# Optimization experiments

Measured on AMD Instinct MI355X. Metric: run time of the kernel, lower is better.

Reference implementation:

```python
import jax, jax.numpy as jnp
import numpy as np


def setup_inputs() -> dict:
    key = jax.random.key(0)
    ks = jax.random.split(key, 5)
    B, T, S = 64, 128, 1024
    IN_DIM, OUT_DIM = 1024, 1024
    decoder_output = jax.random.normal(ks[0], (B, T, OUT_DIM), dtype=jnp.float32)
    encoder_outputs = jax.random.normal(ks[1], (B, S, IN_DIM), dtype=jnp.float32)
    encoder_padding_mask = jax.random.randint(ks[2], (B, S), 0, 2).astype(bool)
    # nn.Linear(output_dim, input_dim, bias=False): weight [input_dim, output_dim]
    W_attn = jax.random.normal(ks[3], (IN_DIM, OUT_DIM), dtype=jnp.float32) * (1.0 / np.sqrt(OUT_DIM))
    # nn.Linear(input_dim+output_dim, output_dim): weight [output_dim, input_dim+output_dim]
    W_out = jax.random.normal(ks[4], (OUT_DIM, IN_DIM + OUT_DIM), dtype=jnp.float32) * (1.0 / np.sqrt(IN_DIM + OUT_DIM))
    b_out = jnp.zeros((OUT_DIM,), dtype=jnp.float32)
    return {"decoder_output": decoder_output, "encoder_outputs": encoder_outputs,
            "encoder_padding_mask": encoder_padding_mask,
            "W_attn": W_attn, "W_out": W_out, "b_out": b_out}


def reference(decoder_output, encoder_outputs, encoder_padding_mask, W_attn, W_out, b_out):
    # general score: bmm(attn(query), key^T)
    q_proj = jnp.einsum('bto,io->bti', decoder_output, W_attn)          # [B,T,in_dim]
    scores = jnp.einsum('bti,bsi->bts', q_proj, encoder_outputs)        # [B,T,S]
    scores = jnp.where(encoder_padding_mask[:, None, :], -jnp.inf, scores)
    attn_weights = jax.nn.softmax(scores, axis=-1)                      # [B,T,S]
    context = jnp.einsum('bts,bsi->bti', attn_weights, encoder_outputs) # [B,T,in_dim]
    cat = jnp.concatenate([context, decoder_output], axis=-1)           # [B,T,in+out]
    attn_outputs = jnp.tanh(jnp.einsum('btc,oc->bto', cat, W_out) + b_out)
    return attn_outputs, attn_weights
```

## Files before the change

kernel.cpp:

```cpp
#include <hip/hip_runtime.h>
#include <math.h>


#define LSTR 40

typedef __attribute__((ext_vector_type(8))) short short8;
typedef __attribute__((ext_vector_type(4))) float f32x4;
typedef __attribute__((ext_vector_type(4))) unsigned short u16x4;

__device__ __forceinline__ unsigned short f2bf(float x) {
    union { float f; unsigned int u; } v; v.f = x;
    unsigned int u = v.u + (0x7fffu + ((v.u >> 16) & 1u));
    return (unsigned short)(u >> 16);
}
__device__ __forceinline__ float bf2f(unsigned short h) {
    union { unsigned int u; float f; } v; v.u = ((unsigned int)h) << 16;
    return v.f;
}

__global__ __launch_bounds__(256) void gemm_bt_split(
    const float* __restrict__ A, const float* __restrict__ B, float* __restrict__ C,
    int N, int K, long long sA, long long sB, long long sC)
{
    const float* Ab = A + blockIdx.z * sA;
    const float* Bb = B + blockIdx.z * sB;
    float*       Cb = C + blockIdx.z * sC;
    const int m0 = blockIdx.x * 128, n0 = blockIdx.y * 128;

    __shared__ unsigned short Ah[128*LSTR], Al[128*LSTR], Bh[128*LSTR], Bl[128*LSTR];

    const int tid = threadIdx.x;
    const int lane = tid & 63, wave = tid >> 6;
    const int wm = (wave & 1) * 64, wn = (wave >> 1) * 64;
    const int fr = lane & 15, kq = lane >> 4;

    f32x4 zero = {0.f, 0.f, 0.f, 0.f};
    f32x4 acc[4][4];
    #pragma unroll
    for (int i = 0; i < 4; i++)
        #pragma unroll
        for (int j = 0; j < 4; j++) acc[i][j] = zero;

    for (int k0 = 0; k0 < K; k0 += 32) {
        #pragma unroll
        for (int i = 0; i < 4; i++) {
            int f = i * 256 + tid;
            int row = f >> 3, c4 = (f & 7) * 4;
            float4 a4 = *(const float4*)(Ab + (long long)(m0 + row) * K + k0 + c4);
            float4 b4 = *(const float4*)(Bb + (long long)(n0 + row) * K + k0 + c4);
            float av[4] = {a4.x, a4.y, a4.z, a4.w};
            float bv[4] = {b4.x, b4.y, b4.z, b4.w};
            u16x4 ah, al, bh, bl;
            #pragma unroll
            for (int j = 0; j < 4; j++) {
                unsigned short h = f2bf(av[j]);
                ah[j] = h; al[j] = f2bf(av[j] - bf2f(h));
                h = f2bf(bv[j]);
                bh[j] = h; bl[j] = f2bf(bv[j] - bf2f(h));
            }
            *(u16x4*)&Ah[row*LSTR + c4] = ah;
            *(u16x4*)&Al[row*LSTR + c4] = al;
            *(u16x4*)&Bh[row*LSTR + c4] = bh;
            *(u16x4*)&Bl[row*LSTR + c4] = bl;
        }
        __syncthreads();

        short8 fah[4], fal[4], fbh[4], fbl[4];
        #pragma unroll
        for (int fi = 0; fi < 4; fi++) {
            fah[fi] = *(const short8*)&Ah[(wm + fi*16 + fr)*LSTR + kq*8];
            fal[fi] = *(const short8*)&Al[(wm + fi*16 + fr)*LSTR + kq*8];
            fbh[fi] = *(const short8*)&Bh[(wn + fi*16 + fr)*LSTR + kq*8];
            fbl[fi] = *(const short8*)&Bl[(wn + fi*16 + fr)*LSTR + kq*8];
        }
        #pragma unroll
        for (int fi = 0; fi < 4; fi++)
            #pragma unroll
            for (int fj = 0; fj < 4; fj++) {
                acc[fi][fj] = __builtin_amdgcn_mfma_f32_16x16x32_bf16(fah[fi], fbh[fj], acc[fi][fj], 0, 0, 0);
                acc[fi][fj] = __builtin_amdgcn_mfma_f32_16x16x32_bf16(fah[fi], fbl[fj], acc[fi][fj], 0, 0, 0);
                acc[fi][fj] = __builtin_amdgcn_mfma_f32_16x16x32_bf16(fal[fi], fbh[fj], acc[fi][fj], 0, 0, 0);
            }
        __syncthreads();
    }

    #pragma unroll
    for (int fi = 0; fi < 4; fi++) {
        int rb = m0 + wm + fi*16 + kq*4;
        #pragma unroll
        for (int fj = 0; fj < 4; fj++) {
            int col = n0 + wn + fj*16 + fr;
            #pragma unroll
            for (int j = 0; j < 4; j++)
                Cb[(long long)(rb + j) * N + col] = acc[fi][fj][j];
        }
    }
}

__global__ __launch_bounds__(256) void softmax_mask(
    float* __restrict__ sw, const int* __restrict__ mask,
    unsigned short* __restrict__ wbf)
{
    const int row = blockIdx.x;
    const int b = row >> 7;
    const int tid = threadIdx.x, lane = tid & 63, wave = tid >> 6;
    float* sr = sw + (long long)row * 1024;
    const int* mr = mask + (long long)b * 1024;

    float4 x = *(const float4*)(sr + tid * 4);
    int4  mk = *(const int4*)(mr + tid * 4);
    float v0 = mk.x ? -INFINITY : x.x;
    float v1 = mk.y ? -INFINITY : x.y;
    float v2 = mk.z ? -INFINITY : x.z;
    float v3 = mk.w ? -INFINITY : x.w;

    float mx = fmaxf(fmaxf(v0, v1), fmaxf(v2, v3));
    #pragma unroll
    for (int off = 32; off; off >>= 1) mx = fmaxf(mx, __shfl_xor(mx, off));
    __shared__ float redm[4];
    __shared__ float reds[4];
    if (lane == 0) redm[wave] = mx;
    __syncthreads();
    mx = fmaxf(fmaxf(redm[0], redm[1]), fmaxf(redm[2], redm[3]));

    float p0 = __expf(v0 - mx), p1 = __expf(v1 - mx);
    float p2 = __expf(v2 - mx), p3 = __expf(v3 - mx);
    float s = (p0 + p1) + (p2 + p3);
    #pragma unroll
    for (int off = 32; off; off >>= 1) s += __shfl_xor(s, off);
    if (lane == 0) reds[wave] = s;
    __syncthreads();
    s = (reds[0] + reds[1]) + (reds[2] + reds[3]);
    float inv = 1.0f / s;

    float w0 = p0*inv, w1 = p1*inv, w2 = p2*inv, w3 = p3*inv;
    float4 w4; w4.x = w0; w4.y = w1; w4.z = w2; w4.w = w3;
    *(float4*)(sr + tid * 4) = w4;
    u16x4 wb; wb[0] = f2bf(w0); wb[1] = f2bf(w1); wb[2] = f2bf(w2); wb[3] = f2bf(w3);
    *(u16x4*)(wbf + (long long)row * 1024 + tid * 4) = wb;
}

__global__ __launch_bounds__(256) void gemm_ctx(
    const unsigned short* __restrict__ Wb, const float* __restrict__ enc,
    unsigned short* __restrict__ cat)
{
    const int bz = blockIdx.z;
    const int n0 = blockIdx.y * 128;
    const unsigned short* Ab = Wb + (long long)bz * 128 * 1024;
    const float* Bb = enc + (long long)bz * 1024 * 1024;

    __shared__ unsigned short Ah[128*LSTR], Bh[128*LSTR];

    const int tid = threadIdx.x, lane = tid & 63, wave = tid >> 6;
    const int wm = (wave & 1) * 64, wn = (wave >> 1) * 64;
    const int fr = lane & 15, kq = lane >> 4;

    f32x4 zero = {0.f, 0.f, 0.f, 0.f};
    f32x4 acc[4][4];
    #pragma unroll
    for (int i = 0; i < 4; i++)
        #pragma unroll
        for (int j = 0; j < 4; j++) acc[i][j] = zero;

    for (int k0 = 0; k0 < 1024; k0 += 32) {
        #pragma unroll
        for (int i = 0; i < 2; i++) {
            int f = i * 256 + tid;
            int row = f >> 2, c8 = (f & 3) * 8;
            *(short8*)&Ah[row*LSTR + c8] = *(const short8*)(Ab + (long long)row*1024 + k0 + c8);
        }
        #pragma unroll
        for (int jj = 0; jj < 16; jj++) {
            int linear = jj * 256 + tid;
            int kr = linear >> 7, n = linear & 127;
            Bh[n*LSTR + kr] = f2bf(Bb[(long long)(k0 + kr) * 1024 + n0 + n]);
        }
        __syncthreads();

        short8 fa[4], fb[4];
        #pragma unroll
        for (int fi = 0; fi < 4; fi++) {
            fa[fi] = *(const short8*)&Ah[(wm + fi*16 + fr)*LSTR + kq*8];
            fb[fi] = *(const short8*)&Bh[(wn + fi*16 + fr)*LSTR + kq*8];
        }
        #pragma unroll
        for (int fi = 0; fi < 4; fi++)
            #pragma unroll
            for (int fj = 0; fj < 4; fj++)
                acc[fi][fj] = __builtin_amdgcn_mfma_f32_16x16x32_bf16(fa[fi], fb[fj], acc[fi][fj], 0, 0, 0);
        __syncthreads();
    }

    #pragma unroll
    for (int fi = 0; fi < 4; fi++) {
        int rb = bz * 128 + wm + fi*16 + kq*4;
        #pragma unroll
        for (int fj = 0; fj < 4; fj++) {
            int col = n0 + wn + fj*16 + fr;
            #pragma unroll
            for (int j = 0; j < 4; j++)
                cat[(long long)(rb + j) * 2048 + col] = f2bf(acc[fi][fj][j]);
        }
    }
}

__global__ __launch_bounds__(256) void pack_dec(
    const float* __restrict__ dec, unsigned short* __restrict__ cat)
{
    long long i = (long long)blockIdx.x * 256 + threadIdx.x;
    float4 x = *(const float4*)(dec + i * 4);
    long long e = i * 4;
    int m = (int)(e >> 10), c = (int)(e & 1023);
    u16x4 h; h[0] = f2bf(x.x); h[1] = f2bf(x.y); h[2] = f2bf(x.z); h[3] = f2bf(x.w);
    *(u16x4*)(cat + (long long)m * 2048 + 1024 + c) = h;
}

__global__ __launch_bounds__(256) void gemm_out(
    const unsigned short* __restrict__ cat, const float* __restrict__ W,
    const float* __restrict__ bias, float* __restrict__ out)
{
    const int m0 = blockIdx.x * 128, n0 = blockIdx.y * 128;

    __shared__ unsigned short Ah[128*LSTR], Bh[128*LSTR];

    const int tid = threadIdx.x, lane = tid & 63, wave = tid >> 6;
    const int wm = (wave & 1) * 64, wn = (wave >> 1) * 64;
    const int fr = lane & 15, kq = lane >> 4;

    f32x4 zero = {0.f, 0.f, 0.f, 0.f};
    f32x4 acc[4][4];
    #pragma unroll
    for (int i = 0; i < 4; i++)
        #pragma unroll
        for (int j = 0; j < 4; j++) acc[i][j] = zero;

    for (int k0 = 0; k0 < 2048; k0 += 32) {
        #pragma unroll
        for (int i = 0; i < 2; i++) {
            int f = i * 256 + tid;
            int row = f >> 2, c8 = (f & 3) * 8;
            *(short8*)&Ah[row*LSTR + c8] = *(const short8*)(cat + (long long)(m0 + row)*2048 + k0 + c8);
        }
        #pragma unroll
        for (int i = 0; i < 4; i++) {
            int f = i * 256 + tid;
            int row = f >> 3, c4 = (f & 7) * 4;
            float4 b4 = *(const float4*)(W + (long long)(n0 + row)*2048 + k0 + c4);
            u16x4 bh; bh[0] = f2bf(b4.x); bh[1] = f2bf(b4.y); bh[2] = f2bf(b4.z); bh[3] = f2bf(b4.w);
            *(u16x4*)&Bh[row*LSTR + c4] = bh;
        }
        __syncthreads();

        short8 fa[4], fb[4];
        #pragma unroll
        for (int fi = 0; fi < 4; fi++) {
            fa[fi] = *(const short8*)&Ah[(wm + fi*16 + fr)*LSTR + kq*8];
            fb[fi] = *(const short8*)&Bh[(wn + fi*16 + fr)*LSTR + kq*8];
        }
        #pragma unroll
        for (int fi = 0; fi < 4; fi++)
            #pragma unroll
            for (int fj = 0; fj < 4; fj++)
                acc[fi][fj] = __builtin_amdgcn_mfma_f32_16x16x32_bf16(fa[fi], fb[fj], acc[fi][fj], 0, 0, 0);
        __syncthreads();
    }

    #pragma unroll
    for (int fi = 0; fi < 4; fi++) {
        int rb = m0 + wm + fi*16 + kq*4;
        #pragma unroll
        for (int fj = 0; fj < 4; fj++) {
            int col = n0 + wn + fj*16 + fr;
            float bb = bias[col];
            #pragma unroll
            for (int j = 0; j < 4; j++)
                out[(long long)(rb + j) * 1024 + col] = tanhf(acc[fi][fj][j] + bb);
        }
    }
}

extern "C" void kernel_launch(void* const* d_in, const int* in_sizes, int n_in,
                              void* d_out, int out_size, void* d_ws, size_t ws_size,
                              hipStream_t stream) {
    const float* dec    = (const float*)d_in[0];
    const float* enc    = (const float*)d_in[1];
    const int*   mask   = (const int*)d_in[2];
    const float* W_attn = (const float*)d_in[3];
    const float* W_out  = (const float*)d_in[4];
    const float* b_out  = (const float*)d_in[5];

    float* out_attn = (float*)d_out;
    float* weights  = out_attn + 8388608;

    char* ws = (char*)d_ws;
    float*          q_proj = (float*)ws;
    unsigned short* w_bf   = (unsigned short*)(ws + (32 << 20));
    unsigned short* cat    = (unsigned short*)(ws + (48 << 20));

    dim3 blk(256);

    gemm_bt_split<<<dim3(64, 8, 1), blk, 0, stream>>>(
        dec, W_attn, q_proj, 1024, 1024, 0, 0, 0);

    gemm_bt_split<<<dim3(1, 8, 64), blk, 0, stream>>>(
        q_proj, enc, weights, 1024, 1024, 128LL*1024, 1024LL*1024, 128LL*1024);

    softmax_mask<<<dim3(8192), blk, 0, stream>>>(weights, mask, w_bf);

    pack_dec<<<dim3(8192), blk, 0, stream>>>(dec, cat);

    gemm_ctx<<<dim3(1, 8, 64), blk, 0, stream>>>(w_bf, enc, cat);

    gemm_out<<<dim3(64, 8, 1), blk, 0, stream>>>(cat, W_out, b_out, out_attn);
}
```

Baseline: 679.3 us.

## Pre-split operands to bf16 hi/lo, use direct global-to-LDS loads, vectorize ctx transpose

Adds separate kernels that convert dec, W_attn and W_out to bf16 (hi/lo pairs where needed) once, so the GEMMs no longer convert inside their K loops. The GEMMs then stage their bf16 tiles with global_load_lds straight into unpadded LDS, and q_proj is stored as bf16 hi/lo instead of fp32. gemm_ctx replaces its scalar transposed encoder loads with float4 loads and a register transpose. gemm_out now reads ctx and dec_hi directly, so the pack_dec kernel is gone. The cost is extra conversion kernels, more workspace traffic, and possible LDS bank conflicts from dropping the row padding.

```diff
diff --git a/kernel.cpp b/kernel.cpp
--- a/kernel.cpp
+++ b/kernel.cpp
@@ -1,8 +1,6 @@
 #include <hip/hip_runtime.h>
 #include <math.h>
 
-
-#define LSTR 40
 
 typedef __attribute__((ext_vector_type(8))) short short8;
 typedef __attribute__((ext_vector_type(4))) float f32x4;
@@ -17,22 +15,50 @@
     union { unsigned int u; float f; } v; v.u = ((unsigned int)h) << 16;
     return v.f;
 }
-
-__global__ __launch_bounds__(256) void gemm_bt_split(
-    const float* __restrict__ A, const float* __restrict__ B, float* __restrict__ C,
-    int N, int K, long long sA, long long sB, long long sC)
-{
-    const float* Ab = A + blockIdx.z * sA;
-    const float* Bb = B + blockIdx.z * sB;
-    float*       Cb = C + blockIdx.z * sC;
+__device__ __forceinline__ void g2lds16(const void* g, void* l) {
+    __builtin_amdgcn_global_load_lds(
+        (const __attribute__((address_space(1))) void*)g,
+        (__attribute__((address_space(3))) void*)l, 16, 0, 0);
+}
+
+__global__ __launch_bounds__(256) void split_f32(
+    const float* __restrict__ src, unsigned short* __restrict__ hi,
+    unsigned short* __restrict__ lo)
+{
+    long long i = (long long)blockIdx.x * 256 + threadIdx.x;
+    float4 x = *(const float4*)(src + i * 4);
+    float v[4] = {x.x, x.y, x.z, x.w};
+    u16x4 h, l;
+    #pragma unroll
+    for (int j = 0; j < 4; j++) {
+        h[j] = f2bf(v[j]);
+        l[j] = f2bf(v[j] - bf2f(h[j]));
+    }
+    *(u16x4*)(hi + i * 4) = h;
+    *(u16x4*)(lo + i * 4) = l;
+}
+
+__global__ __launch_bounds__(256) void cvt_f32(
+    const float* __restrict__ src, unsigned short* __restrict__ dst)
+{
+    long long i = (long long)blockIdx.x * 256 + threadIdx.x;
+    float4 x = *(const float4*)(src + i * 4);
+    u16x4 h; h[0] = f2bf(x.x); h[1] = f2bf(x.y); h[2] = f2bf(x.z); h[3] = f2bf(x.w);
+    *(u16x4*)(dst + i * 4) = h;
+}
+
+__global__ __launch_bounds__(256) void gemm3_qproj(
+    const unsigned short* __restrict__ Ahi, const unsigned short* __restrict__ Alo,
+    const unsigned short* __restrict__ Bhi, const unsigned short* __restrict__ Blo,
+    unsigned short* __restrict__ Chi, unsigned short* __restrict__ Clo)
+{
     const int m0 = blockIdx.x * 128, n0 = blockIdx.y * 128;
-
-    __shared__ unsigned short Ah[128*LSTR], Al[128*LSTR], Bh[128*LSTR], Bl[128*LSTR];
-
-    const int tid = threadIdx.x;
-    const int lane = tid & 63, wave = tid >> 6;
+    __shared__ __align__(16) unsigned short Ah[128*32], Al[128*32], Bh[128*32], Bl[128*32];
+
+    const int tid = threadIdx.x, lane = tid & 63, wave = tid >> 6;
     const int wm = (wave & 1) * 64, wn = (wave >> 1) * 64;
     const int fr = lane & 15, kq = lane >> 4;
+    const int row0 = tid >> 2, c80 = (tid & 3) * 8;
 
     f32x4 zero = {0.f, 0.f, 0.f, 0.f};
     f32x4 acc[4][4];
@@ -41,37 +67,28 @@
         #pragma unroll
         for (int j = 0; j < 4; j++) acc[i][j] = zero;
 
-    for (int k0 = 0; k0 < K; k0 += 32) {
-        #pragma unroll
-        for (int i = 0; i < 4; i++) {
-            int f = i * 256 + tid;
-            int row = f >> 3, c4 = (f & 7) * 4;
-            float4 a4 = *(const float4*)(Ab + (long long)(m0 + row) * K + k0 + c4);
-            float4 b4 = *(const float4*)(Bb + (long long)(n0 + row) * K + k0 + c4);
-            float av[4] = {a4.x, a4.y, a4.z, a4.w};
-            float bv[4] = {b4.x, b4.y, b4.z, b4.w};
-            u16x4 ah, al, bh, bl;
-            #pragma unroll
-            for (int j = 0; j < 4; j++) {
-                unsigned short h = f2bf(av[j]);
-                ah[j] = h; al[j] = f2bf(av[j] - bf2f(h));
-                h = f2bf(bv[j]);
-                bh[j] = h; bl[j] = f2bf(bv[j] - bf2f(h));
-            }
-            *(u16x4*)&Ah[row*LSTR + c4] = ah;
-            *(u16x4*)&Al[row*LSTR + c4] = al;
-            *(u16x4*)&Bh[row*LSTR + c4] = bh;
-            *(u16x4*)&Bl[row*LSTR + c4] = bl;
-        }
+    for (int k0 = 0; k0 < 1024; k0 += 32) {
+        const unsigned short* pa = Ahi + (long long)(m0 + row0) * 1024 + k0 + c80;
+        const unsigned short* pl = Alo + (long long)(m0 + row0) * 1024 + k0 + c80;
+        const unsigned short* pb = Bhi + (long long)(n0 + row0) * 1024 + k0 + c80;
+        const unsigned short* pm = Blo + (long long)(n0 + row0) * 1024 + k0 + c80;
+        g2lds16(pa,            &Ah[tid*8]);
+        g2lds16(pa + 64*1024,  &Ah[tid*8 + 2048]);
+        g2lds16(pl,            &Al[tid*8]);
+        g2lds16(pl + 64*1024,  &Al[tid*8 + 2048]);
+        g2lds16(pb,            &Bh[tid*8]);
+        g2lds16(pb + 64*1024,  &Bh[tid*8 + 2048]);
+        g2lds16(pm,            &Bl[tid*8]);
+        g2lds16(pm + 64*1024,  &Bl[tid*8 + 2048]);
         __syncthreads();
 
         short8 fah[4], fal[4], fbh[4], fbl[4];
         #pragma unroll
         for (int fi = 0; fi < 4; fi++) {
-            fah[fi] = *(const short8*)&Ah[(wm + fi*16 + fr)*LSTR + kq*8];
-            fal[fi] = *(const short8*)&Al[(wm + fi*16 + fr)*LSTR + kq*8];
-            fbh[fi] = *(const short8*)&Bh[(wn + fi*16 + fr)*LSTR + kq*8];
-            fbl[fi] = *(const short8*)&Bl[(wn + fi*16 + fr)*LSTR + kq*8];
+            fah[fi] = *(const short8*)&Ah[(wm + fi*16 + fr)*32 + kq*8];
+            fal[fi] = *(const short8*)&Al[(wm + fi*16 + fr)*32 + kq*8];
+            fbh[fi] = *(const short8*)&Bh[(wn + fi*16 + fr)*32 + kq*8];
+            fbl[fi] = *(const short8*)&Bl[(wn + fi*16 + fr)*32 + kq*8];
         }
         #pragma unroll
         for (int fi = 0; fi < 4; fi++)
@@ -91,8 +108,93 @@
         for (int fj = 0; fj < 4; fj++) {
             int col = n0 + wn + fj*16 + fr;
             #pragma unroll
+            for (int j = 0; j < 4; j++) {
+                float x = acc[fi][fj][j];
+                unsigned short h = f2bf(x);
+                Chi[(long long)(rb + j) * 1024 + col] = h;
+                Clo[(long long)(rb + j) * 1024 + col] = f2bf(x - bf2f(h));
+            }
+        }
+    }
+}
+
+__global__ __launch_bounds__(256) void gemm3_scores(
+    const unsigned short* __restrict__ Qhi, const unsigned short* __restrict__ Qlo,
+    const float* __restrict__ enc, float* __restrict__ C)
+{
+    const int bz = blockIdx.z, n0 = blockIdx.y * 128;
+    const unsigned short* Ahb = Qhi + (long long)bz * 128 * 1024;
+    const unsigned short* Alb = Qlo + (long long)bz * 128 * 1024;
+    const float* Bb = enc + (long long)bz * 1024 * 1024;
+    float* Cb = C + (long long)bz * 128 * 1024;
+
+    __shared__ __align__(16) unsigned short Ah[128*32], Al[128*32], Bh[128*32], Bl[128*32];
+
+    const int tid = threadIdx.x, lane = tid & 63, wave = tid >> 6;
+    const int wm = (wave & 1) * 64, wn = (wave >> 1) * 64;
+    const int fr = lane & 15, kq = lane >> 4;
+    const int row0 = tid >> 2, c80 = (tid & 3) * 8;
+
+    f32x4 zero = {0.f, 0.f, 0.f, 0.f};
+    f32x4 acc[4][4];
+    #pragma unroll
+    for (int i = 0; i < 4; i++)
+        #pragma unroll
+        for (int j = 0; j < 4; j++) acc[i][j] = zero;
+
+    for (int k0 = 0; k0 < 1024; k0 += 32) {
+        const unsigned short* pa = Ahb + (long long)row0 * 1024 + k0 + c80;
+        const unsigned short* pl = Alb + (long long)row0 * 1024 + k0 + c80;
+        g2lds16(pa,           &Ah[tid*8]);
+        g2lds16(pa + 64*1024, &Ah[tid*8 + 2048]);
+        g2lds16(pl,           &Al[tid*8]);
+        g2lds16(pl + 64*1024, &Al[tid*8 + 2048]);
+
+        #pragma unroll
+        for (int i = 0; i < 4; i++) {
+            int u = i * 256 + tid;
+            int row = u >> 3, c4 = (u & 7) * 4;
+            float4 b4 = *(const float4*)(Bb + (long long)(n0 + row) * 1024 + k0 + c4);
+            float bv[4] = {b4.x, b4.y, b4.z, b4.w};
+            u16x4 hh, ll;
+            #pragma unroll
+            for (int j = 0; j < 4; j++) {
+                hh[j] = f2bf(bv[j]);
+                ll[j] = f2bf(bv[j] - bf2f(hh[j]));
+            }
+            *(u16x4*)&Bh[row*32 + c4] = hh;
+            *(u16x4*)&Bl[row*32 + c4] = ll;
+        }
+        __syncthreads();
+
+        short8 fah[4], fal[4], fbh[4], fbl[4];
+        #pragma unroll
+        for (int fi = 0; fi < 4; fi++) {
+            fah[fi] = *(const short8*)&Ah[(wm + fi*16 + fr)*32 + kq*8];
+            fal[fi] = *(const short8*)&Al[(wm + fi*16 + fr)*32 + kq*8];
+            fbh[fi] = *(const short8*)&Bh[(wn + fi*16 + fr)*32 + kq*8];
+            fbl[fi] = *(const short8*)&Bl[(wn + fi*16 + fr)*32 + kq*8];
+        }
+        #pragma unroll
+        for (int fi = 0; fi < 4; fi++)
+            #pragma unroll
+            for (int fj = 0; fj < 4; fj++) {
+                acc[fi][fj] = __builtin_amdgcn_mfma_f32_16x16x32_bf16(fah[fi], fbh[fj], acc[fi][fj], 0, 0, 0);
+                acc[fi][fj] = __builtin_amdgcn_mfma_f32_16x16x32_bf16(fah[fi], fbl[fj], acc[fi][fj], 0, 0, 0);
+                acc[fi][fj] = __builtin_amdgcn_mfma_f32_16x16x32_bf16(fal[fi], fbh[fj], acc[fi][fj], 0, 0, 0);
+            }
+        __syncthreads();
+    }
+
+    #pragma unroll
+    for (int fi = 0; fi < 4; fi++) {
+        int rb = wm + fi*16 + kq*4;
+        #pragma unroll
+        for (int fj = 0; fj < 4; fj++) {
+            int col = n0 + wn + fj*16 + fr;
+            #pragma unroll
             for (int j = 0; j < 4; j++)
-                Cb[(long long)(rb + j) * N + col] = acc[fi][fj][j];
+                Cb[(long long)(rb + j) * 1024 + col] = acc[fi][fj][j];
         }
     }
 }
@@ -117,8 +219,7 @@
     float mx = fmaxf(fmaxf(v0, v1), fmaxf(v2, v3));
     #pragma unroll
     for (int off = 32; off; off >>= 1) mx = fmaxf(mx, __shfl_xor(mx, off));
-    __shared__ float redm[4];
-    __shared__ float reds[4];
+    __shared__ float redm[4], reds[4];
     if (lane == 0) redm[wave] = mx;
     __syncthreads();
     mx = fmaxf(fmaxf(redm[0], redm[1]), fmaxf(redm[2], redm[3]));
@@ -140,20 +241,23 @@
     *(u16x4*)(wbf + (long long)row * 1024 + tid * 4) = wb;
 }
 
+#define BSTR 40
 __global__ __launch_bounds__(256) void gemm_ctx(
     const unsigned short* __restrict__ Wb, const float* __restrict__ enc,
-    unsigned short* __restrict__ cat)
-{
-    const int bz = blockIdx.z;
-    const int n0 = blockIdx.y * 128;
+    unsigned short* __restrict__ ctx)
+{
+    const int bz = blockIdx.z, n0 = blockIdx.y * 128;
     const unsigned short* Ab = Wb + (long long)bz * 128 * 1024;
     const float* Bb = enc + (long long)bz * 1024 * 1024;
 
-    __shared__ unsigned short Ah[128*LSTR], Bh[128*LSTR];
+    __shared__ __align__(16) unsigned short Ah[128*32];
+    __shared__ __align__(16) unsigned short Bt[128*BSTR];
 
     const int tid = threadIdx.x, lane = tid & 63, wave = tid >> 6;
     const int wm = (wave & 1) * 64, wn = (wave >> 1) * 64;
     const int fr = lane & 15, kq = lane >> 4;
+    const int row0 = tid >> 2, c80 = (tid & 3) * 8;
+    const int kb = tid & 7, nb = tid >> 3;
 
     f32x4 zero = {0.f, 0.f, 0.f, 0.f};
     f32x4 acc[4][4];
@@ -163,25 +267,30 @@
         for (int j = 0; j < 4; j++) acc[i][j] = zero;
 
     for (int k0 = 0; k0 < 1024; k0 += 32) {
-        #pragma unroll
-        for (int i = 0; i < 2; i++) {
-            int f = i * 256 + tid;
-            int row = f >> 2, c8 = (f & 3) * 8;
-            *(short8*)&Ah[row*LSTR + c8] = *(const short8*)(Ab + (long long)row*1024 + k0 + c8);
-        }
-        #pragma unroll
-        for (int jj = 0; jj < 16; jj++) {
-            int linear = jj * 256 + tid;
-            int kr = linear >> 7, n = linear & 127;
-            Bh[n*LSTR + kr] = f2bf(Bb[(long long)(k0 + kr) * 1024 + n0 + n]);
-        }
+        const unsigned short* pa = Ab + (long long)row0 * 1024 + k0 + c80;
+        g2lds16(pa,           &Ah[tid*8]);
+        g2lds16(pa + 64*1024, &Ah[tid*8 + 2048]);
+
+        float4 r0 = *(const float4*)(Bb + (long long)(k0 + kb*4 + 0) * 1024 + n0 + nb*4);
+        float4 r1 = *(const float4*)(Bb + (long long)(k0 + kb*4 + 1) * 1024 + n0 + nb*4);
+        float4 r2 = *(const float4*)(Bb + (long long)(k0 + kb*4 + 2) * 1024 + n0 + nb*4);
+        float4 r3 = *(const float4*)(Bb + (long long)(k0 + kb*4 + 3) * 1024 + n0 + nb*4);
+        u16x4 v;
+        v[0] = f2bf(r0.x); v[1] = f2bf(r1.x); v[2] = f2bf(r2.x); v[3] = f2bf(r3.x);
+        *(u16x4*)&Bt[(nb*4 + 0)*BSTR + kb*4] = v;
+        v[0] = f2bf(r0.y); v[1] = f2bf(r1.y); v[2] = f2bf(r2.y); v[3] = f2bf(r3.y);
+        *(u16x4*)&Bt[(nb*4 + 1)*BSTR + kb*4] = v;
+        v[0] = f2bf(r0.z); v[1] = f2bf(r1.z); v[2] = f2bf(r2.z); v[3] = f2bf(r3.z);
+        *(u16x4*)&Bt[(nb*4 + 2)*BSTR + kb*4] = v;
+        v[0] = f2bf(r0.w); v[1] = f2bf(r1.w); v[2] = f2bf(r2.w); v[3] = f2bf(r3.w);
+        *(u16x4*)&Bt[(nb*4 + 3)*BSTR + kb*4] = v;
         __syncthreads();
 
         short8 fa[4], fb[4];
         #pragma unroll
         for (int fi = 0; fi < 4; fi++) {
-            fa[fi] = *(const short8*)&Ah[(wm + fi*16 + fr)*LSTR + kq*8];
-            fb[fi] = *(const short8*)&Bh[(wn + fi*16 + fr)*LSTR + kq*8];
+            fa[fi] = *(const short8*)&Ah[(wm + fi*16 + fr)*32 + kq*8];
+            fb[fi] = *(const short8*)&Bt[(wn + fi*16 + fr)*BSTR + kq*8];
         }
         #pragma unroll
         for (int fi = 0; fi < 4; fi++)
@@ -199,33 +308,23 @@
             int col = n0 + wn + fj*16 + fr;
             #pragma unroll
             for (int j = 0; j < 4; j++)
-                cat[(long long)(rb + j) * 2048 + col] = f2bf(acc[fi][fj][j]);
-        }
-    }
-}
-
-__global__ __launch_bounds__(256) void pack_dec(
-    const float* __restrict__ dec, unsigned short* __restrict__ cat)
-{
-    long long i = (long long)blockIdx.x * 256 + threadIdx.x;
-    float4 x = *(const float4*)(dec + i * 4);
-    long long e = i * 4;
-    int m = (int)(e >> 10), c = (int)(e & 1023);
-    u16x4 h; h[0] = f2bf(x.x); h[1] = f2bf(x.y); h[2] = f2bf(x.z); h[3] = f2bf(x.w);
-    *(u16x4*)(cat + (long long)m * 2048 + 1024 + c) = h;
+                ctx[(long long)(rb + j) * 1024 + col] = f2bf(acc[fi][fj][j]);
+        }
+    }
 }
 
 __global__ __launch_bounds__(256) void gemm_out(
-    const unsigned short* __restrict__ cat, const float* __restrict__ W,
-    const float* __restrict__ bias, float* __restrict__ out)
+    const unsigned short* __restrict__ ctx, const unsigned short* __restrict__ dech,
+    const unsigned short* __restrict__ Wb, const float* __restrict__ bias,
+    float* __restrict__ out)
 {
     const int m0 = blockIdx.x * 128, n0 = blockIdx.y * 128;
-
-    __shared__ unsigned short Ah[128*LSTR], Bh[128*LSTR];
+    __shared__ __align__(16) unsigned short Ah[128*32], Bh[128*32];
 
     const int tid = threadIdx.x, lane = tid & 63, wave = tid >> 6;
     const int wm = (wave & 1) * 64, wn = (wave >> 1) * 64;
     const int fr = lane & 15, kq = lane >> 4;
+    const int row0 = tid >> 2, c80 = (tid & 3) * 8;
 
     f32x4 zero = {0.f, 0.f, 0.f, 0.f};
     f32x4 acc[4][4];
@@ -235,27 +334,21 @@
         for (int j = 0; j < 4; j++) acc[i][j] = zero;
 
     for (int k0 = 0; k0 < 2048; k0 += 32) {
-        #pragma unroll
-        for (int i = 0; i < 2; i++) {
-            int f = i * 256 + tid;
-            int row = f >> 2, c8 = (f & 3) * 8;
-            *(short8*)&Ah[row*LSTR + c8] = *(const short8*)(cat + (long long)(m0 + row)*2048 + k0 + c8);
-        }
-        #pragma unroll
-        for (int i = 0; i < 4; i++) {
-            int f = i * 256 + tid;
-            int row = f >> 3, c4 = (f & 7) * 4;
-            float4 b4 = *(const float4*)(W + (long long)(n0 + row)*2048 + k0 + c4);
-            u16x4 bh; bh[0] = f2bf(b4.x); bh[1] = f2bf(b4.y); bh[2] = f2bf(b4.z); bh[3] = f2bf(b4.w);
-            *(u16x4*)&Bh[row*LSTR + c4] = bh;
-        }
+        const unsigned short* As = (k0 < 1024) ? ctx : dech;
+        int kk = k0 & 1023;
+        const unsigned short* pa = As + (long long)(m0 + row0) * 1024 + kk + c80;
+        const unsigned short* pb = Wb + (long long)(n0 + row0) * 2048 + k0 + c80;
+        g2lds16(pa,           &Ah[tid*8]);
+        g2lds16(pa + 64*1024, &Ah[tid*8 + 2048]);
+        g2lds16(pb,           &Bh[tid*8]);
+        g2lds16(pb + 64*2048, &Bh[tid*8 + 2048]);
         __syncthreads();
 
         short8 fa[4], fb[4];
         #pragma unroll
         for (int fi = 0; fi < 4; fi++) {
-            fa[fi] = *(const short8*)&Ah[(wm + fi*16 + fr)*LSTR + kq*8];
-            fb[fi] = *(const short8*)&Bh[(wn + fi*16 + fr)*LSTR + kq*8];
+            fa[fi] = *(const short8*)&Ah[(wm + fi*16 + fr)*32 + kq*8];
+            fb[fi] = *(const short8*)&Bh[(wn + fi*16 + fr)*32 + kq*8];
         }
         #pragma unroll
         for (int fi = 0; fi < 4; fi++)
@@ -293,23 +386,25 @@
     float* weights  = out_attn + 8388608;
 
     char* ws = (char*)d_ws;
-    float*          q_proj = (float*)ws;
-    unsigned short* w_bf   = (unsigned short*)(ws + (32 << 20));
-    unsigned short* cat    = (unsigned short*)(ws + (48 << 20));
+    unsigned short* dec_hi = (unsigned short*)(ws);
+    unsigned short* dec_lo = (unsigned short*)(ws + (16 << 20));
+    unsigned short* wa_hi  = (unsigned short*)(ws + (32 << 20));
+    unsigned short* wa_lo  = (unsigned short*)(ws + (34 << 20));
+    unsigned short* wout_b = (unsigned short*)(ws + (36 << 20));
+    unsigned short* q_hi   = (unsigned short*)(ws + (40 << 20));
+    unsigned short* q_lo   = (unsigned short*)(ws + (56 << 20));
+    unsigned short* w_bf   = (unsigned short*)(ws + (72 << 20));
+    unsigned short* ctx_bf = (unsigned short*)(ws + (88 << 20));
 
     dim3 blk(256);
 
-    gemm_bt_split<<<dim3(64, 8, 1), blk, 0, stream>>>(
-        dec, W_attn, q_proj, 1024, 1024, 0, 0, 0);
-
-    gemm_bt_split<<<dim3(1, 8, 64), blk, 0, stream>>>(
-        q_proj, enc, weights, 1024, 1024, 128LL*1024, 1024LL*1024, 128LL*1024);
-
+    split_f32<<<dim3(8192), blk, 0, stream>>>(dec, dec_hi, dec_lo);
+    split_f32<<<dim3(1024), blk, 0, stream>>>(W_attn, wa_hi, wa_lo);
+    cvt_f32<<<dim3(2048), blk, 0, stream>>>(W_out, wout_b);
+
+    gemm3_qproj<<<dim3(64, 8, 1), blk, 0, stream>>>(dec_hi, dec_lo, wa_hi, wa_lo, q_hi, q_lo);
+    gemm3_scores<<<dim3(1, 8, 64), blk, 0, stream>>>(q_hi, q_lo, enc, weights);
     softmax_mask<<<dim3(8192), blk, 0, stream>>>(weights, mask, w_bf);
-
-    pack_dec<<<dim3(8192), blk, 0, stream>>>(dec, cat);
-
-    gemm_ctx<<<dim3(1, 8, 64), blk, 0, stream>>>(w_bf, enc, cat);
-
-    gemm_out<<<dim3(64, 8, 1), blk, 0, stream>>>(cat, W_out, b_out, out_attn);
-}
+    gemm_ctx<<<dim3(1, 8, 64), blk, 0, stream>>>(w_bf, enc, ctx_bf);
+    gemm_out<<<dim3(64, 8, 1), blk, 0, stream>>>(ctx_bf, dec_hi, wout_b, b_out, out_attn);
+}
```

New measurement: 647.3 us. 1.05x faster.
